# Performance work log

Measured on AMD Instinct MI355X. Metric: run time of the kernel, lower is better.

Reference implementation:

```python
import jax, jax.numpy as jnp
import numpy as np

D_MODEL = 1024
H = 16
D_K = D_MODEL // H
NEG = -1.0e9


def setup_inputs() -> dict:
    key = jax.random.key(0)
    ks = jax.random.split(key, 12)
    B, S = 2, 2048
    s = 1.0 / np.sqrt(D_MODEL)
    inp = {
        "q": jax.random.normal(ks[0], (B, S, D_MODEL), jnp.float32),
        "k": jax.random.normal(ks[1], (B, S, D_MODEL), jnp.float32),
        "v": jax.random.normal(ks[2], (B, S, D_MODEL), jnp.float32),
        "mask": jnp.tril(jnp.ones((S, S), jnp.int32))[None, None, :, :],
        "wq": jax.random.normal(ks[3], (D_MODEL, D_MODEL), jnp.float32) * s,
        "bq": jax.random.normal(ks[4], (D_MODEL,), jnp.float32) * s,
        "wk": jax.random.normal(ks[5], (D_MODEL, D_MODEL), jnp.float32) * s,
        "bk": jax.random.normal(ks[6], (D_MODEL,), jnp.float32) * s,
        "wv": jax.random.normal(ks[7], (D_MODEL, D_MODEL), jnp.float32) * s,
        "bv": jax.random.normal(ks[8], (D_MODEL,), jnp.float32) * s,
        "wo": jax.random.normal(ks[9], (D_MODEL, D_MODEL), jnp.float32) * s,
        "bo": jax.random.normal(ks[10], (D_MODEL,), jnp.float32) * s,
    }
    return inp


def _split_heads(x):
    # [B,S,D] -> [B,H,S,d_k]
    B, S, _ = x.shape
    return x.reshape(B, S, H, D_K).transpose(0, 2, 1, 3)


def reference(q, k, v, mask, wq, bq, wk, bk, wv, bv, wo, bo):
    # torch Linear: y = x @ W.T + b
    query = _split_heads(q @ wq.T + bq)
    key = _split_heads(k @ wk.T + bk)
    value = _split_heads(v @ wv.T + bv)
    # scores: [B,H,S,S]
    scores = jnp.einsum("bhqd,bhkd->bhqk", query, key) / jnp.sqrt(
        jnp.asarray(D_K, query.dtype))
    scores = jnp.where(mask == 0, jnp.asarray(NEG, scores.dtype), scores)
    attn = jax.nn.softmax(scores, axis=-1)  # dropout p=0.0 -> identity
    x = jnp.einsum("bhqk,bhkd->bhqd", attn, value)
    B, _, S, _ = x.shape
    x = x.transpose(0, 2, 1, 3).reshape(B, S, D_MODEL)
    return x @ wo.T + bo
```

## Files before the change

kernel.cpp:

```cpp
#include <hip/hip_runtime.h>
#include <hip/hip_bf16.h>
#include <cstdint>
#include <cstddef>

#define BATCH 2
#define SEQ   2048
#define DM    1024
#define NH    16
#define DK    64
#define MROWS (BATCH*SEQ)

typedef __bf16 bf16;
typedef float  f32x4  __attribute__((ext_vector_type(4)));
typedef bf16   bf16x8 __attribute__((ext_vector_type(8)));
typedef bf16   bf16x4 __attribute__((ext_vector_type(4)));

#define MFMA32(a, b, c) __builtin_amdgcn_mfma_f32_16x16x32_bf16(a, b, c, 0, 0, 0)

__device__ __forceinline__ void llds16(const void* gc, void* l) {
    void* g = (void*)gc;
    __builtin_amdgcn_global_load_lds(
        (__attribute__((address_space(1))) uint32_t*)g,
        (__attribute__((address_space(3))) uint32_t*)l,
        16, 0, 0);
}

__global__ __launch_bounds__(256) void k_convert(
    const float* __restrict__ q, const float* __restrict__ k, const float* __restrict__ v,
    const float* __restrict__ wq, const float* __restrict__ wk, const float* __restrict__ wv,
    const float* __restrict__ wo,
    bf16* __restrict__ qb, bf16* __restrict__ kb, bf16* __restrict__ vb,
    bf16* __restrict__ wqb, bf16* __restrict__ wkb, bf16* __restrict__ wvb,
    bf16* __restrict__ wob) {
    long t = (long)blockIdx.x * blockDim.x + threadIdx.x;
    const long NQ = (long)MROWS * DM / 4;
    const long NW = (long)DM * DM / 4;
    const float* src; bf16* dst; long off;
    if (t < NQ)            { src = q;  dst = qb;  off = t; }
    else if (t < 2*NQ)     { src = k;  dst = kb;  off = t - NQ; }
    else if (t < 3*NQ)     { src = v;  dst = vb;  off = t - 2*NQ; }
    else {
        long u = t - 3*NQ;
        if (u < NW)        { src = wq; dst = wqb; off = u; }
        else if (u < 2*NW) { src = wk; dst = wkb; off = u - NW; }
        else if (u < 3*NW) { src = wv; dst = wvb; off = u - 2*NW; }
        else               { src = wo; dst = wob; off = u - 3*NW; }
    }
    f32x4 x = *(const f32x4*)(src + off * 4);
    bf16x4 y;
    y[0] = (bf16)x[0]; y[1] = (bf16)x[1]; y[2] = (bf16)x[2]; y[3] = (bf16)x[3];
    *(bf16x4*)(dst + off * 4) = y;
}

__global__ __launch_bounds__(256) void k_gemm_qkv(
    const bf16* __restrict__ qb, const bf16* __restrict__ kb, const bf16* __restrict__ vb,
    const bf16* __restrict__ wqb, const bf16* __restrict__ wkb, const bf16* __restrict__ wvb,
    const float* __restrict__ bq, const float* __restrict__ bk, const float* __restrict__ bv,
    bf16* __restrict__ Qf, bf16* __restrict__ Kf, bf16* __restrict__ Vf) {
    const int z = blockIdx.z;
    const int bid = blockIdx.x;
    const bf16* A; const bf16* B; const float* bias;
    int m0, n0;
    if (z == 2) {
        A = vb; B = wvb; bias = bv;
        m0 = (bid >> 4) * 128;
        n0 = (bid & 15) * 64;
    } else {
        A = z ? wkb : wqb; B = z ? kb : qb; bias = z ? bk : bq;
        m0 = (bid >> 6) * 128;
        n0 = (bid & 63) * 64;
    }

    constexpr int K = DM, BK = 32;
    __shared__ bf16 sA[128 * BK];
    __shared__ bf16 sB[64 * BK];
    const int tid = threadIdx.x;
    const int l = tid & 63, w = tid >> 6;
    const int quad = l >> 4, l15 = l & 15;
    const int wm = w & 1, wn = w >> 1;
    const int srow = l >> 2, scol = (l & 3) * 8;

    f32x4 acc[4][2] = {};
    for (int k0 = 0; k0 < K; k0 += BK) {
#pragma unroll
        for (int i = 0; i < 2; ++i) {
            int r16 = w * 32 + i * 16;
            llds16(A + (size_t)(m0 + r16 + srow) * K + k0 + scol, &sA[r16 * BK]);
        }
        llds16(B + (size_t)(n0 + w * 16 + srow) * K + k0 + scol, &sB[w * 16 * BK]);
        __syncthreads();

        bf16x8 af[4], bfr[2];
#pragma unroll
        for (int mi = 0; mi < 4; ++mi)
            af[mi] = *(const bf16x8*)&sA[(wm * 64 + mi * 16 + l15) * BK + quad * 8];
#pragma unroll
        for (int ni = 0; ni < 2; ++ni)
            bfr[ni] = *(const bf16x8*)&sB[(wn * 32 + ni * 16 + l15) * BK + quad * 8];
#pragma unroll
        for (int mi = 0; mi < 4; ++mi)
#pragma unroll
            for (int ni = 0; ni < 2; ++ni)
                acc[mi][ni] = MFMA32(af[mi], bfr[ni], acc[mi][ni]);
        __syncthreads();
    }

    if (z == 2) {
#pragma unroll
        for (int ni = 0; ni < 2; ++ni) {
            int dcol = n0 + wn * 32 + ni * 16 + l15;
            int hh2 = dcol >> 6;
            int dtile = (dcol >> 4) & 3;
            float bias_v = bias[dcol];
#pragma unroll
            for (int mi = 0; mi < 4; ++mi) {
                int srw = m0 + wm * 64 + mi * 16;
                int bb = srw >> 11, sl = srw & 2047;
                int kc = sl >> 5;
                bf16x4 pack;
#pragma unroll
                for (int r = 0; r < 4; ++r)
                    pack[r] = (bf16)(acc[mi][ni][r] + bias_v);
                size_t entry = ((size_t)(bb * NH + hh2) * 64 + kc) * 4 + dtile;
                *(bf16x4*)(Vf + entry * 512 + (size_t)(quad * 16 + l15) * 8 + (mi & 1) * 4) = pack;
            }
        }
    } else {
        bf16* out = z ? Kf : Qf;
        const float scale = z ? 1.0f : 0.18033688f;
        float bias_rv[4][4];
#pragma unroll
        for (int mi = 0; mi < 4; ++mi)
#pragma unroll
            for (int r = 0; r < 4; ++r)
                bias_rv[mi][r] = bias[m0 + wm * 64 + mi * 16 + quad * 4 + r];
#pragma unroll
        for (int ni = 0; ni < 2; ++ni) {
            int scolg = n0 + wn * 32 + ni * 16 + l15;
            int bb = scolg >> 11, s = scolg & 2047;
            int s16 = s >> 4;
#pragma unroll
            for (int mi = 0; mi < 4; ++mi) {
                int drow = m0 + wm * 64 + mi * 16;
                int hh2 = (drow >> 6) & 15;
                int chunk = (drow & 63) >> 5;
                int qp = 2 * (mi & 1) + (quad >> 1);
                bf16x4 pack;
#pragma unroll
                for (int r = 0; r < 4; ++r)
                    pack[r] = (bf16)((acc[mi][ni][r] + bias_rv[mi][r]) * scale);
                size_t entry = ((size_t)(bb * NH + hh2) * 128 + s16) * 2 + chunk;
                *(bf16x4*)(out + entry * 512 + (size_t)(qp * 16 + l15) * 8 + (quad & 1) * 4) = pack;
            }
        }
    }
}

__global__ __launch_bounds__(256) void k_gemm_out(
    const bf16* __restrict__ X, const bf16* __restrict__ wob,
    const float* __restrict__ bo, float* __restrict__ out) {
    constexpr int K = DM, BK = 32, NS = K / BK;
    const int m0 = blockIdx.y * 128, n0 = blockIdx.x * 64;
    __shared__ bf16 sA[2][128 * BK];
    __shared__ bf16 sB[2][64 * BK];
    const int tid = threadIdx.x;
    const int l = tid & 63, w = tid >> 6;
    const int quad = l >> 4, l15 = l & 15;
    const int wm = w & 1, wn = w >> 1;
    const int srow = l >> 2, scol = (l & 3) * 8;

#pragma unroll
    for (int i = 0; i < 2; ++i) {
        int r16 = w * 32 + i * 16;
        llds16(X + (size_t)(m0 + r16 + srow) * K + scol, &sA[0][r16 * BK]);
    }
    llds16(wob + (size_t)(n0 + w * 16 + srow) * K + scol, &sB[0][w * 16 * BK]);

    f32x4 acc[4][2] = {};
    for (int s = 0; s < NS; ++s) {
        __syncthreads();
        const int cur = s & 1;
        if (s + 1 < NS) {
            const int k0 = (s + 1) * BK;
#pragma unroll
            for (int i = 0; i < 2; ++i) {
                int r16 = w * 32 + i * 16;
                llds16(X + (size_t)(m0 + r16 + srow) * K + k0 + scol, &sA[cur ^ 1][r16 * BK]);
            }
            llds16(wob + (size_t)(n0 + w * 16 + srow) * K + k0 + scol, &sB[cur ^ 1][w * 16 * BK]);
        }

        bf16x8 af[4], bfr[2];
#pragma unroll
        for (int mi = 0; mi < 4; ++mi)
            af[mi] = *(const bf16x8*)&sA[cur][(wm * 64 + mi * 16 + l15) * BK + quad * 8];
#pragma unroll
        for (int ni = 0; ni < 2; ++ni)
            bfr[ni] = *(const bf16x8*)&sB[cur][(wn * 32 + ni * 16 + l15) * BK + quad * 8];
#pragma unroll
        for (int mi = 0; mi < 4; ++mi)
#pragma unroll
            for (int ni = 0; ni < 2; ++ni)
                acc[mi][ni] = MFMA32(af[mi], bfr[ni], acc[mi][ni]);
    }
#pragma unroll
    for (int mi = 0; mi < 4; ++mi)
#pragma unroll
        for (int ni = 0; ni < 2; ++ni) {
            int col = n0 + wn * 32 + ni * 16 + l15;
            float bias_v = bo[col];
            int rbase = m0 + wm * 64 + mi * 16 + quad * 4;
#pragma unroll
            for (int r = 0; r < 4; ++r)
                out[(size_t)(rbase + r) * DM + col] = acc[mi][ni][r] + bias_v;
        }
}

__global__ __launch_bounds__(256, 4) void k_flash(const bf16* __restrict__ Qf,
                                                  const bf16* __restrict__ Kf,
                                                  const bf16* __restrict__ Vf,
                                                  bf16* __restrict__ X) {
    const int bh = blockIdx.x;
    const int qt = 31 - (int)blockIdx.y;
    const int b = bh >> 4, h = bh & 15;
    const int tid = threadIdx.x, w = tid >> 6, l = tid & 63;
    const int quad = l >> 4, l15 = l & 15;
    __shared__ bf16 sKV[2][16 * 512];

    const bf16* qfp = Qf + (size_t)bh * 128 * 1024;
    const bf16* kfp = Kf + (size_t)bh * 128 * 1024;
    const bf16* vfp = Vf + (size_t)bh * 64 * 4 * 512;

    const int qt16 = qt * 4 + w;
    const int qglob = qt16 * 16 + l15;

    bf16x8 qf[2];
#pragma unroll
    for (int c = 0; c < 2; ++c)
        qf[c] = *(const bf16x8*)(qfp + ((size_t)qt16 * 2 + c) * 512 + (size_t)l * 8);

    f32x4 o[4] = {};
    float lp = 0.f;

#pragma unroll
    for (int i = 0; i < 4; ++i) {
        int e = w * 4 + i;
        const bf16* src = (e < 8) ? kfp + ((size_t)e) * 512
                                  : vfp + ((size_t)(e - 8)) * 512;
        llds16(src + (size_t)l * 8, &sKV[0][e * 512]);
    }

    for (int j = 0; j <= qt; ++j) {
        __syncthreads();
        const bf16* cur = sKV[j & 1];
        if (j < qt) {
            int j1 = j + 1;
#pragma unroll
            for (int i = 0; i < 4; ++i) {
                int e = w * 4 + i;
                const bf16* src = (e < 8) ? kfp + ((size_t)(j1 * 8 + e)) * 512
                                          : vfp + ((size_t)(j1 * 8 + (e - 8))) * 512;
                llds16(src + (size_t)l * 8, (void*)&sKV[j1 & 1][e * 512]);
            }
        }

        f32x4 st[4];
#pragma unroll
        for (int ni = 0; ni < 4; ++ni) {
            bf16x8 k0 = *(const bf16x8*)&cur[(size_t)(ni * 2 + 0) * 512 + l * 8];
            bf16x8 k1 = *(const bf16x8*)&cur[(size_t)(ni * 2 + 1) * 512 + l * 8];
            f32x4 zz = {};
            zz = MFMA32(k0, qf[0], zz);
            st[ni] = MFMA32(k1, qf[1], zz);
        }

        const bool diag = (j == qt);
#pragma unroll
        for (int c = 0; c < 2; ++c) {
            bf16x8 pb;
#pragma unroll
            for (int half = 0; half < 2; ++half) {
                int ni = 2 * c + half;
#pragma unroll
                for (int r = 0; r < 4; ++r) {
                    float s = st[ni][r];
                    if (diag) {
                        int key = j * 64 + ni * 16 + quad * 4 + r;
                        if (key > qglob) s = -1e30f;
                    }
                    float e = __builtin_amdgcn_exp2f(s);
                    lp += e;
                    pb[half * 4 + r] = (bf16)e;
                }
            }
#pragma unroll
            for (int dt = 0; dt < 4; ++dt) {
                bf16x8 vv = *(const bf16x8*)&cur[(size_t)(8 + c * 4 + dt) * 512 + l * 8];
                o[dt] = MFMA32(vv, pb, o[dt]);
            }
        }
    }

    lp += __shfl_xor(lp, 16, 64);
    lp += __shfl_xor(lp, 32, 64);
    float rv = 1.f / lp;

    __syncthreads();
    bf16* Xw = &sKV[0][w * 16 * 72];
#pragma unroll
    for (int dt = 0; dt < 4; ++dt) {
        bf16x4 pk;
#pragma unroll
        for (int r = 0; r < 4; ++r)
            pk[r] = (bf16)(o[dt][r] * rv);
        *(bf16x4*)&Xw[l15 * 72 + dt * 16 + quad * 4] = pk;
    }
#pragma unroll
    for (int i = 0; i < 2; ++i) {
        int row = i * 8 + (l >> 3);
        bf16x8 vv = *(const bf16x8*)&Xw[row * 72 + (l & 7) * 8];
        *(bf16x8*)(X + (size_t)(b * SEQ + qt16 * 16 + row) * DM + h * 64 + (l & 7) * 8) = vv;
    }
}

extern "C" void kernel_launch(void* const* d_in, const int* in_sizes, int n_in,
                              void* d_out, int out_size, void* d_ws, size_t ws_size,
                              hipStream_t stream) {
    const float* q  = (const float*)d_in[0];
    const float* k  = (const float*)d_in[1];
    const float* v  = (const float*)d_in[2];
    const float* wq = (const float*)d_in[4];
    const float* bq = (const float*)d_in[5];
    const float* wk = (const float*)d_in[6];
    const float* bk = (const float*)d_in[7];
    const float* wv = (const float*)d_in[8];
    const float* bv = (const float*)d_in[9];
    const float* wo = (const float*)d_in[10];
    const float* bo = (const float*)d_in[11];
    float* out = (float*)d_out;

    uint8_t* ws = (uint8_t*)d_ws;
    const size_t SZ_ACT = (size_t)MROWS * DM * sizeof(bf16);
    const size_t SZ_W   = (size_t)DM * DM * sizeof(bf16);
    bf16* qb  = (bf16*)(ws);
    bf16* kb  = (bf16*)(ws + SZ_ACT);
    bf16* vb  = (bf16*)(ws + 2 * SZ_ACT);
    bf16* wqb = (bf16*)(ws + 3 * SZ_ACT);
    bf16* wkb = (bf16*)(ws + 3 * SZ_ACT + SZ_W);
    bf16* wvb = (bf16*)(ws + 3 * SZ_ACT + 2 * SZ_W);
    bf16* wob = (bf16*)(ws + 3 * SZ_ACT + 3 * SZ_W);
    bf16* Qf  = (bf16*)(ws + 3 * SZ_ACT + 4 * SZ_W);
    bf16* Kf  = (bf16*)(ws + 4 * SZ_ACT + 4 * SZ_W);
    bf16* Vf  = (bf16*)(ws + 5 * SZ_ACT + 4 * SZ_W);
    bf16* X   = (bf16*)(ws + 6 * SZ_ACT + 4 * SZ_W);

    {
        long total_vec4 = 3L * MROWS * DM / 4 + 4L * DM * DM / 4;
        k_convert<<<dim3((unsigned)(total_vec4 / 256)), 256, 0, stream>>>(
            q, k, v, wq, wk, wv, wo, qb, kb, vb, wqb, wkb, wvb, wob);
    }
    k_gemm_qkv<<<dim3(512, 1, 3), 256, 0, stream>>>(
        qb, kb, vb, wqb, wkb, wvb, bq, bk, bv, Qf, Kf, Vf);
    k_flash<<<dim3(BATCH * NH, SEQ / 64), 256, 0, stream>>>(Qf, Kf, Vf, X);
    k_gemm_out<<<dim3(DM / 64, MROWS / 128), 256, 0, stream>>>(X, wob, bo, out);
}
```

Baseline: 226.6 us.

## Load K/V fragments directly from global memory in flash kernel, dropping LDS staging

The flash-attention kernel no longer stages each K/V tile into double-buffered shared memory with global_load_lds plus a block barrier per iteration. Instead, each wave reads its MFMA operand fragments straight from global memory into registers, relying on L2/L1 for reuse across the four waves. This removes the per-iteration __syncthreads and the LDS round trip, but drops the explicit prefetch overlap and makes every wave fetch the same K/V data, raising global/cache traffic and register pressure.

After: 245.3 us. +8.3%, slower.

```diff
diff --git a/kernel.cpp b/kernel.cpp
--- a/kernel.cpp
+++ b/kernel.cpp
@@ -225,7 +225,7 @@
     const int b = bh >> 4, h = bh & 15;
     const int tid = threadIdx.x, w = tid >> 6, l = tid & 63;
     const int quad = l >> 4, l15 = l & 15;
-    __shared__ bf16 sKV[2][16 * 512];
+    __shared__ bf16 Xs[4 * 16 * 72];
 
     const bf16* qfp = Qf + (size_t)bh * 128 * 1024;
     const bf16* kfp = Kf + (size_t)bh * 128 * 1024;
@@ -242,36 +242,24 @@
     f32x4 o[4] = {};
     float lp = 0.f;
 
-#pragma unroll
-    for (int i = 0; i < 4; ++i) {
-        int e = w * 4 + i;
-        const bf16* src = (e < 8) ? kfp + ((size_t)e) * 512
-                                  : vfp + ((size_t)(e - 8)) * 512;
-        llds16(src + (size_t)l * 8, &sKV[0][e * 512]);
-    }
+    const bf16* kbase = kfp + (size_t)l * 8;
+    const bf16* vbase = vfp + (size_t)l * 8;
 
     for (int j = 0; j <= qt; ++j) {
-        __syncthreads();
-        const bf16* cur = sKV[j & 1];
-        if (j < qt) {
-            int j1 = j + 1;
-#pragma unroll
-            for (int i = 0; i < 4; ++i) {
-                int e = w * 4 + i;
-                const bf16* src = (e < 8) ? kfp + ((size_t)(j1 * 8 + e)) * 512
-                                          : vfp + ((size_t)(j1 * 8 + (e - 8))) * 512;
-                llds16(src + (size_t)l * 8, (void*)&sKV[j1 & 1][e * 512]);
-            }
-        }
+        const bf16* kj = kbase + (size_t)(j * 8) * 512;
+        const bf16* vj = vbase + (size_t)(j * 8) * 512;
+
+        bf16x8 kv[8];
+#pragma unroll
+        for (int e = 0; e < 8; ++e)
+            kv[e] = *(const bf16x8*)(kj + (size_t)e * 512);
 
         f32x4 st[4];
 #pragma unroll
         for (int ni = 0; ni < 4; ++ni) {
-            bf16x8 k0 = *(const bf16x8*)&cur[(size_t)(ni * 2 + 0) * 512 + l * 8];
-            bf16x8 k1 = *(const bf16x8*)&cur[(size_t)(ni * 2 + 1) * 512 + l * 8];
             f32x4 zz = {};
-            zz = MFMA32(k0, qf[0], zz);
-            st[ni] = MFMA32(k1, qf[1], zz);
+            zz = MFMA32(kv[2 * ni], qf[0], zz);
+            st[ni] = MFMA32(kv[2 * ni + 1], qf[1], zz);
         }
 
         const bool diag = (j == qt);
@@ -295,7 +283,7 @@
             }
 #pragma unroll
             for (int dt = 0; dt < 4; ++dt) {
-                bf16x8 vv = *(const bf16x8*)&cur[(size_t)(8 + c * 4 + dt) * 512 + l * 8];
+                bf16x8 vv = *(const bf16x8*)(vj + (size_t)(c * 4 + dt) * 512);
                 o[dt] = MFMA32(vv, pb, o[dt]);
             }
         }
@@ -305,8 +293,7 @@
     lp += __shfl_xor(lp, 32, 64);
     float rv = 1.f / lp;
 
-    __syncthreads();
-    bf16* Xw = &sKV[0][w * 16 * 72];
+    bf16* Xw = &Xs[w * 16 * 72];
 #pragma unroll
     for (int dt = 0; dt < 4; ++dt) {
         bf16x4 pk;
@@ -315,6 +302,7 @@
             pk[r] = (bf16)(o[dt][r] * rv);
         *(bf16x4*)&Xw[l15 * 72 + dt * 16 + quad * 4] = pk;
     }
+    __syncthreads();
 #pragma unroll
     for (int i = 0; i < 2; ++i) {
         int row = i * 8 + (l >> 3);
```

## Double GEMM K-tile to 64 and XOR-swizzle LDS layout in projection GEMMs

Applied to the files above, without the earlier changes.

Raises the K-step from 32 to 64 in both the QKV projection GEMM and the output projection GEMM, which halves the number of loop iterations and barriers. The shared-memory layout now uses an XOR swizzle of the 16-byte chunk index by the row so that fragment reads avoid LDS bank conflicts. LDS use per block doubles, which may lower occupancy, especially for the double-buffered output GEMM.

New measurement: 208.2 us. 8.1% less time.

```diff
diff --git a/kernel.cpp b/kernel.cpp
--- a/kernel.cpp
+++ b/kernel.cpp
@@ -71,37 +71,51 @@
         n0 = (bid & 63) * 64;
     }
 
-    constexpr int K = DM, BK = 32;
+    constexpr int K = DM, BK = 64;
     __shared__ bf16 sA[128 * BK];
     __shared__ bf16 sB[64 * BK];
     const int tid = threadIdx.x;
     const int l = tid & 63, w = tid >> 6;
     const int quad = l >> 4, l15 = l & 15;
     const int wm = w & 1, wn = w >> 1;
-    const int srow = l >> 2, scol = (l & 3) * 8;
+    const int srow = l >> 3;
+    const int scol = ((l & 7) ^ srow) * 8;
 
     f32x4 acc[4][2] = {};
     for (int k0 = 0; k0 < K; k0 += BK) {
 #pragma unroll
+        for (int i = 0; i < 4; ++i) {
+            int r8 = w * 32 + i * 8;
+            llds16(A + (size_t)(m0 + r8 + srow) * K + k0 + scol, &sA[r8 * BK]);
+        }
+#pragma unroll
         for (int i = 0; i < 2; ++i) {
-            int r16 = w * 32 + i * 16;
-            llds16(A + (size_t)(m0 + r16 + srow) * K + k0 + scol, &sA[r16 * BK]);
-        }
-        llds16(B + (size_t)(n0 + w * 16 + srow) * K + k0 + scol, &sB[w * 16 * BK]);
+            int r8 = w * 16 + i * 8;
+            llds16(B + (size_t)(n0 + r8 + srow) * K + k0 + scol, &sB[r8 * BK]);
+        }
         __syncthreads();
 
-        bf16x8 af[4], bfr[2];
-#pragma unroll
-        for (int mi = 0; mi < 4; ++mi)
-            af[mi] = *(const bf16x8*)&sA[(wm * 64 + mi * 16 + l15) * BK + quad * 8];
-#pragma unroll
-        for (int ni = 0; ni < 2; ++ni)
-            bfr[ni] = *(const bf16x8*)&sB[(wn * 32 + ni * 16 + l15) * BK + quad * 8];
-#pragma unroll
-        for (int mi = 0; mi < 4; ++mi)
-#pragma unroll
-            for (int ni = 0; ni < 2; ++ni)
-                acc[mi][ni] = MFMA32(af[mi], bfr[ni], acc[mi][ni]);
+#pragma unroll
+        for (int kk = 0; kk < 2; ++kk) {
+            bf16x8 af[4], bfr[2];
+#pragma unroll
+            for (int mi = 0; mi < 4; ++mi) {
+                int row = wm * 64 + mi * 16 + l15;
+                int byt = (row * 128 + kk * 64 + quad * 16) ^ ((row & 7) << 4);
+                af[mi] = *(const bf16x8*)((const char*)sA + byt);
+            }
+#pragma unroll
+            for (int ni = 0; ni < 2; ++ni) {
+                int row = wn * 32 + ni * 16 + l15;
+                int byt = (row * 128 + kk * 64 + quad * 16) ^ ((row & 7) << 4);
+                bfr[ni] = *(const bf16x8*)((const char*)sB + byt);
+            }
+#pragma unroll
+            for (int mi = 0; mi < 4; ++mi)
+#pragma unroll
+                for (int ni = 0; ni < 2; ++ni)
+                    acc[mi][ni] = MFMA32(af[mi], bfr[ni], acc[mi][ni]);
+        }
         __syncthreads();
     }
 
@@ -159,7 +173,7 @@
 __global__ __launch_bounds__(256) void k_gemm_out(
     const bf16* __restrict__ X, const bf16* __restrict__ wob,
     const float* __restrict__ bo, float* __restrict__ out) {
-    constexpr int K = DM, BK = 32, NS = K / BK;
+    constexpr int K = DM, BK = 64, NS = K / BK;
     const int m0 = blockIdx.y * 128, n0 = blockIdx.x * 64;
     __shared__ bf16 sA[2][128 * BK];
     __shared__ bf16 sB[2][64 * BK];
@@ -167,14 +181,19 @@
     const int l = tid & 63, w = tid >> 6;
     const int quad = l >> 4, l15 = l & 15;
     const int wm = w & 1, wn = w >> 1;
-    const int srow = l >> 2, scol = (l & 3) * 8;
-
+    const int srow = l >> 3;
+    const int scol = ((l & 7) ^ srow) * 8;
+
+#pragma unroll
+    for (int i = 0; i < 4; ++i) {
+        int r8 = w * 32 + i * 8;
+        llds16(X + (size_t)(m0 + r8 + srow) * K + scol, &sA[0][r8 * BK]);
+    }
 #pragma unroll
     for (int i = 0; i < 2; ++i) {
-        int r16 = w * 32 + i * 16;
-        llds16(X + (size_t)(m0 + r16 + srow) * K + scol, &sA[0][r16 * BK]);
-    }
-    llds16(wob + (size_t)(n0 + w * 16 + srow) * K + scol, &sB[0][w * 16 * BK]);
+        int r8 = w * 16 + i * 8;
+        llds16(wob + (size_t)(n0 + r8 + srow) * K + scol, &sB[0][r8 * BK]);
+    }
 
     f32x4 acc[4][2] = {};
     for (int s = 0; s < NS; ++s) {
@@ -183,25 +202,38 @@
         if (s + 1 < NS) {
             const int k0 = (s + 1) * BK;
 #pragma unroll
+            for (int i = 0; i < 4; ++i) {
+                int r8 = w * 32 + i * 8;
+                llds16(X + (size_t)(m0 + r8 + srow) * K + k0 + scol, &sA[cur ^ 1][r8 * BK]);
+            }
+#pragma unroll
             for (int i = 0; i < 2; ++i) {
-                int r16 = w * 32 + i * 16;
-                llds16(X + (size_t)(m0 + r16 + srow) * K + k0 + scol, &sA[cur ^ 1][r16 * BK]);
-            }
-            llds16(wob + (size_t)(n0 + w * 16 + srow) * K + k0 + scol, &sB[cur ^ 1][w * 16 * BK]);
-        }
-
-        bf16x8 af[4], bfr[2];
-#pragma unroll
-        for (int mi = 0; mi < 4; ++mi)
-            af[mi] = *(const bf16x8*)&sA[cur][(wm * 64 + mi * 16 + l15) * BK + quad * 8];
-#pragma unroll
-        for (int ni = 0; ni < 2; ++ni)
-            bfr[ni] = *(const bf16x8*)&sB[cur][(wn * 32 + ni * 16 + l15) * BK + quad * 8];
-#pragma unroll
-        for (int mi = 0; mi < 4; ++mi)
-#pragma unroll
-            for (int ni = 0; ni < 2; ++ni)
-                acc[mi][ni] = MFMA32(af[mi], bfr[ni], acc[mi][ni]);
+                int r8 = w * 16 + i * 8;
+                llds16(wob + (size_t)(n0 + r8 + srow) * K + k0 + scol, &sB[cur ^ 1][r8 * BK]);
+            }
+        }
+
+#pragma unroll
+        for (int kk = 0; kk < 2; ++kk) {
+            bf16x8 af[4], bfr[2];
+#pragma unroll
+            for (int mi = 0; mi < 4; ++mi) {
+                int row = wm * 64 + mi * 16 + l15;
+                int byt = (row * 128 + kk * 64 + quad * 16) ^ ((row & 7) << 4);
+                af[mi] = *(const bf16x8*)((const char*)&sA[cur][0] + byt);
+            }
+#pragma unroll
+            for (int ni = 0; ni < 2; ++ni) {
+                int row = wn * 32 + ni * 16 + l15;
+                int byt = (row * 128 + kk * 64 + quad * 16) ^ ((row & 7) << 4);
+                bfr[ni] = *(const bf16x8*)((const char*)&sB[cur][0] + byt);
+            }
+#pragma unroll
+            for (int mi = 0; mi < 4; ++mi)
+#pragma unroll
+                for (int ni = 0; ni < 2; ++ni)
+                    acc[mi][ni] = MFMA32(af[mi], bfr[ni], acc[mi][ni]);
+        }
     }
 #pragma unroll
     for (int mi = 0; mi < 4; ++mi)
```
